# Performance work log

Measured on AMD Instinct MI355X. Metric: run time of the kernel, lower is better.

Reference implementation:

```python
import jax, jax.numpy as jnp
import numpy as np

B, S, H = 4, 1024, 1024
NH = 16
DH = H // NH  # 64


def setup_inputs() -> dict:
    key = jax.random.key(0)
    ks = jax.random.split(key, 8)
    std = 1.0 / np.sqrt(H)
    return {
        "query": jax.random.normal(ks[0], (B, S, H), jnp.float32),
        "key": jax.random.normal(ks[1], (B, S, H), jnp.float32),
        "value": jax.random.normal(ks[2], (B, S, H), jnp.float32),
        "masks": jnp.ones((B, S), jnp.float32),
        "Wq": jax.random.normal(ks[3], (H, H), jnp.float32) * std,
        "bq": jnp.zeros((H,), jnp.float32),
        "Wk": jax.random.normal(ks[4], (H, H), jnp.float32) * std,
        "bk": jnp.zeros((H,), jnp.float32),
        "Wv": jax.random.normal(ks[5], (H, H), jnp.float32) * std,
        "bv": jnp.zeros((H,), jnp.float32),
    }


def reference(query, key, value, masks, Wq, bq, Wk, bk, Wv, bv):
    # ReLU-gated projections (torch Linear: x @ W.T + b)
    qp = jax.nn.relu(jnp.einsum("bsh,oh->bso", query, Wq) + bq)
    kp = jax.nn.relu(jnp.einsum("bsh,oh->bso", key, Wk) + bk)
    vp = jax.nn.relu(jnp.einsum("bsh,oh->bso", value, Wv) + bv)
    # chunk(dim=2)+cat(dim=0) == split hidden into (NH, DH) contiguous slices
    qh = qp.reshape(B, S, NH, DH)
    kh = kp.reshape(B, S, NH, DH)
    vh = vp.reshape(B, S, NH, DH)
    scale = 1.0 / jnp.sqrt(jnp.asarray(DH, qp.dtype))
    # [B, NH, Sq, Sk]
    alpha = jnp.einsum("bqnd,bknd->bnqk", qh, kh) * scale
    alpha = jax.nn.softmax(alpha, axis=-1)
    # post-softmax multiplicative mask, applied per QUERY position
    alpha = alpha * masks[:, None, :, None]
    hiddens = jnp.einsum("bnqk,bknd->bqnd", alpha, vh).reshape(B, S, H)
    return hiddens + query
```

## Files before the change

### kernel.cpp

```cpp
#include <hip/hip_runtime.h>


typedef __attribute__((ext_vector_type(8))) __bf16 bf16x8;
typedef __attribute__((ext_vector_type(4))) float f32x4;
typedef __attribute__((ext_vector_type(8))) unsigned short u16x8;
typedef __attribute__((ext_vector_type(4))) unsigned short u16x4;

#define XQ_OFF 0u
#define XK_OFF 4194304u
#define XV_OFF 8388608u
#define WQ_OFF 12582912u
#define WK_OFF 13631488u
#define WV_OFF 14680064u
#define QP_OFF 15728640u
#define KP_OFF 19922944u
#define VP_OFF 24117248u
#define VT_OFF 28311552u

__device__ __forceinline__ unsigned short f2bf(float f) {
  union { float f; unsigned int u; } c; c.f = f;
  return (unsigned short)((c.u + 0x7fffu + ((c.u >> 16) & 1u)) >> 16);
}

__global__ __launch_bounds__(256) void cvt_kernel(
    const float* __restrict__ q, const float* __restrict__ k, const float* __restrict__ v,
    const float* __restrict__ wq, const float* __restrict__ wk, const float* __restrict__ wv,
    unsigned short* __restrict__ ws) {
  const int z = blockIdx.y;
  const float* src; unsigned short* dst; int n;
  switch (z) {
    case 0: src = q;  dst = ws + XQ_OFF; n = 4194304; break;
    case 1: src = k;  dst = ws + XK_OFF; n = 4194304; break;
    case 2: src = v;  dst = ws + XV_OFF; n = 4194304; break;
    case 3: src = wq; dst = ws + WQ_OFF; n = 1048576; break;
    case 4: src = wk; dst = ws + WK_OFF; n = 1048576; break;
    default: src = wv; dst = ws + WV_OFF; n = 1048576; break;
  }
  const int i8 = (blockIdx.x * 256 + threadIdx.x) * 8;
  if (i8 >= n) return;
  const float4 f0 = *(const float4*)(src + i8);
  const float4 f1 = *(const float4*)(src + i8 + 4);
  u16x8 r;
  r[0] = f2bf(f0.x); r[1] = f2bf(f0.y); r[2] = f2bf(f0.z); r[3] = f2bf(f0.w);
  r[4] = f2bf(f1.x); r[5] = f2bf(f1.y); r[6] = f2bf(f1.z); r[7] = f2bf(f1.w);
  *(u16x8*)(dst + i8) = r;
}

__global__ __launch_bounds__(256) void proj_gemm(
    unsigned short* __restrict__ ws,
    const float* __restrict__ bq, const float* __restrict__ bk, const float* __restrict__ bv) {
  __shared__ unsigned short As[128 * 32];
  __shared__ unsigned short Bs[128 * 32];
  const int z = blockIdx.z;
  const unsigned short* X = ws + (z == 0 ? XQ_OFF : z == 1 ? XK_OFF : XV_OFF);
  const unsigned short* W = ws + (z == 0 ? WQ_OFF : z == 1 ? WK_OFF : WV_OFF);
  unsigned short* P = ws + (z == 0 ? QP_OFF : z == 1 ? KP_OFF : VP_OFF);
  const float* bias = z == 0 ? bq : z == 1 ? bk : bv;

  const int tid  = threadIdx.x;
  const int lane = tid & 63;
  const int w    = tid >> 6;
  const int quad = lane >> 4;
  const int l15  = lane & 15;
  const int wr = w >> 1, wc = w & 1;
  const int m0 = blockIdx.y * 128;
  const int n0 = blockIdx.x * 128;

  f32x4 acc[4][4];
#pragma unroll
  for (int i = 0; i < 4; ++i)
#pragma unroll
    for (int j = 0; j < 4; ++j) acc[i][j] = f32x4{0.f, 0.f, 0.f, 0.f};

  for (int kt = 0; kt < 32; ++kt) {
    const int k0 = kt * 32;
#pragma unroll
    for (int pass = 0; pass < 2; ++pass) {
      const int c   = pass * 256 + tid;
      const int row = c >> 2;
      const int kc  = (c & 3) * 8;
      const unsigned short* ga = X + (size_t)(m0 + row) * 1024 + k0 + kc;
      const unsigned short* gb = W + (size_t)(n0 + row) * 1024 + k0 + kc;
      unsigned short* la = &As[(pass * 256 + w * 64) * 8];
      unsigned short* lb = &Bs[(pass * 256 + w * 64) * 8];
      __builtin_amdgcn_global_load_lds((const __attribute__((address_space(1))) void*)ga,
                                       (__attribute__((address_space(3))) void*)la, 16, 0, 0);
      __builtin_amdgcn_global_load_lds((const __attribute__((address_space(1))) void*)gb,
                                       (__attribute__((address_space(3))) void*)lb, 16, 0, 0);
    }
    __syncthreads();
    bf16x8 af[4], bfv[4];
#pragma unroll
    for (int mi = 0; mi < 4; ++mi)
      af[mi] = *(const bf16x8*)&As[(wr * 64 + mi * 16 + l15) * 32 + quad * 8];
#pragma unroll
    for (int ni = 0; ni < 4; ++ni)
      bfv[ni] = *(const bf16x8*)&Bs[(wc * 64 + ni * 16 + l15) * 32 + quad * 8];
#pragma unroll
    for (int mi = 0; mi < 4; ++mi)
#pragma unroll
      for (int ni = 0; ni < 4; ++ni)
        acc[mi][ni] = __builtin_amdgcn_mfma_f32_16x16x32_bf16(af[mi], bfv[ni], acc[mi][ni], 0, 0, 0);
    __syncthreads();
  }
#pragma unroll
  for (int mi = 0; mi < 4; ++mi)
#pragma unroll
    for (int ni = 0; ni < 4; ++ni) {
      const int col = n0 + wc * 64 + ni * 16 + l15;
      const float bvv = bias[col];
      const int row0 = m0 + wr * 64 + mi * 16 + quad * 4;
#pragma unroll
      for (int r = 0; r < 4; ++r) {
        float v = acc[mi][ni][r] + bvv;
        v = v > 0.f ? v : 0.f;
        P[(size_t)(row0 + r) * 1024 + col] = f2bf(v);
      }
    }
}

__global__ __launch_bounds__(256) void vtrans_kernel(
    const unsigned short* __restrict__ VP, unsigned short* __restrict__ VT) {
  __shared__ unsigned short T[64 * 72];
  const int tid = threadIdx.x;
  const int bh = blockIdx.y;
  const int b = bh >> 4, h = bh & 15;
  const int s0 = blockIdx.x * 64;
  const int rr = tid >> 2;
  const int cc = (tid & 3) * 16;
  {
    const unsigned short* g = &VP[(size_t)(b * 1024 + s0 + rr) * 1024 + h * 64 + cc];
    *(u16x8*)&T[rr * 72 + cc]     = *(const u16x8*)g;
    *(u16x8*)&T[rr * 72 + cc + 8] = *(const u16x8*)(g + 8);
  }
  __syncthreads();
  {
    unsigned short o[16];
#pragma unroll
    for (int jj = 0; jj < 16; ++jj) {
      const int j = (jj + (tid & 3) * 4) & 15;
      o[j] = T[(cc + j) * 72 + rr];
    }
    unsigned short* g = &VT[(size_t)(bh * 64 + rr) * 1024 + s0 + cc];
    *(u16x8*)g       = *(const u16x8*)&o[0];
    *(u16x8*)(g + 8) = *(const u16x8*)&o[8];
  }
}

__global__ __launch_bounds__(256, 2) void attn_kernel(
    const unsigned short* __restrict__ QP, const unsigned short* __restrict__ KP,
    const unsigned short* __restrict__ VT, const float* __restrict__ masks,
    const float* __restrict__ query, float* __restrict__ out) {
  __shared__ unsigned short Kt[64 * 72];
  __shared__ unsigned short Vt[64 * 72];
  __shared__ unsigned short Pl[4][32 * 72];
  const int tid  = threadIdx.x;
  const int lane = tid & 63;
  const int w    = tid >> 6;
  const int quad = lane >> 4;
  const int l15  = lane & 15;
  const int b = blockIdx.z, h = blockIdx.y;
  const int q0w = blockIdx.x * 128 + w * 32;
  const size_t base = (size_t)b * 1024 * 1024;
  const int bh = b * 16 + h;

  bf16x8 qf[2][2];
#pragma unroll
  for (int mt = 0; mt < 2; ++mt)
#pragma unroll
    for (int kk = 0; kk < 2; ++kk)
      qf[mt][kk] = *(const bf16x8*)&QP[base + (size_t)(q0w + mt * 16 + l15) * 1024 +
                                       h * 64 + kk * 32 + quad * 8];

  f32x4 o[2][4];
  float lsum[2][4];
#pragma unroll
  for (int mt = 0; mt < 2; ++mt)
#pragma unroll
    for (int nd = 0; nd < 4; ++nd) o[mt][nd] = f32x4{0.f, 0.f, 0.f, 0.f};
#pragma unroll
  for (int mt = 0; mt < 2; ++mt)
#pragma unroll
    for (int r = 0; r < 4; ++r) lsum[mt][r] = 0.f;

  const int srow = tid >> 2;
  const int c0   = (tid & 3) * 16;
  const float cvt = 0.18033688011112042f;

  for (int kb = 0; kb < 16; ++kb) {
    const int key0 = kb * 64;
    {
      const unsigned short* gk = &KP[base + (size_t)(key0 + srow) * 1024 + h * 64 + c0];
      *(u16x8*)&Kt[srow * 72 + c0]     = *(const u16x8*)gk;
      *(u16x8*)&Kt[srow * 72 + c0 + 8] = *(const u16x8*)(gk + 8);
      const unsigned short* gv = &VT[(size_t)(bh * 64 + srow) * 1024 + key0 + c0];
      *(u16x8*)&Vt[srow * 72 + c0]     = *(const u16x8*)gv;
      *(u16x8*)&Vt[srow * 72 + c0 + 8] = *(const u16x8*)(gv + 8);
    }
    __syncthreads();

#pragma unroll
    for (int mt = 0; mt < 2; ++mt) {
      f32x4 s[4];
#pragma unroll
      for (int ni = 0; ni < 4; ++ni) s[ni] = f32x4{0.f, 0.f, 0.f, 0.f};
#pragma unroll
      for (int kk = 0; kk < 2; ++kk)
#pragma unroll
        for (int ni = 0; ni < 4; ++ni) {
          bf16x8 kf = *(const bf16x8*)&Kt[(ni * 16 + l15) * 72 + kk * 32 + quad * 8];
          s[ni] = __builtin_amdgcn_mfma_f32_16x16x32_bf16(qf[mt][kk], kf, s[ni], 0, 0, 0);
        }
#pragma unroll
      for (int ni = 0; ni < 4; ++ni)
#pragma unroll
        for (int r = 0; r < 4; ++r) {
          const float p = exp2f(s[ni][r] * cvt - 8.0f);
          Pl[w][(mt * 16 + quad * 4 + r) * 72 + ni * 16 + l15] = f2bf(p);
          lsum[mt][r] += p;
        }
    }

#pragma unroll
    for (int kk = 0; kk < 2; ++kk) {
      bf16x8 pa[2];
#pragma unroll
      for (int mt = 0; mt < 2; ++mt)
        pa[mt] = *(const bf16x8*)&Pl[w][(mt * 16 + l15) * 72 + kk * 32 + quad * 8];
#pragma unroll
      for (int nd = 0; nd < 4; ++nd) {
        bf16x8 vf = *(const bf16x8*)&Vt[(nd * 16 + l15) * 72 + kk * 32 + quad * 8];
#pragma unroll
        for (int mt = 0; mt < 2; ++mt)
          o[mt][nd] = __builtin_amdgcn_mfma_f32_16x16x32_bf16(pa[mt], vf, o[mt][nd], 0, 0, 0);
      }
    }
    __syncthreads();
  }

#pragma unroll
  for (int mt = 0; mt < 2; ++mt) {
#pragma unroll
    for (int r = 0; r < 4; ++r) {
      float rs = lsum[mt][r];
      rs += __shfl_xor(rs, 1);
      rs += __shfl_xor(rs, 2);
      rs += __shfl_xor(rs, 4);
      rs += __shfl_xor(rs, 8);
      const int row = q0w + mt * 16 + quad * 4 + r;
      const float scale = masks[b * 1024 + row] / rs;
#pragma unroll
      for (int nd = 0; nd < 4; ++nd) {
        const int col = h * 64 + nd * 16 + l15;
        const size_t gi = base + (size_t)row * 1024 + col;
        out[gi] = o[mt][nd][r] * scale + query[gi];
      }
    }
  }
}

extern "C" void kernel_launch(void* const* d_in, const int* in_sizes, int n_in,
                              void* d_out, int out_size, void* d_ws, size_t ws_size,
                              hipStream_t stream) {
  const float* q     = (const float*)d_in[0];
  const float* k     = (const float*)d_in[1];
  const float* v     = (const float*)d_in[2];
  const float* masks = (const float*)d_in[3];
  const float* Wq    = (const float*)d_in[4];
  const float* bq    = (const float*)d_in[5];
  const float* Wk    = (const float*)d_in[6];
  const float* bk    = (const float*)d_in[7];
  const float* Wv    = (const float*)d_in[8];
  const float* bv    = (const float*)d_in[9];
  float* out = (float*)d_out;
  unsigned short* ws = (unsigned short*)d_ws;

  cvt_kernel<<<dim3(2048, 6), 256, 0, stream>>>(q, k, v, Wq, Wk, Wv, ws);
  proj_gemm<<<dim3(8, 32, 3), 256, 0, stream>>>(ws, bq, bk, bv);
  vtrans_kernel<<<dim3(16, 64), 256, 0, stream>>>(ws + VP_OFF, ws + VT_OFF);
  attn_kernel<<<dim3(8, 16, 4), 256, 0, stream>>>(ws + QP_OFF, ws + KP_OFF, ws + VT_OFF,
                                                  masks, q, out);
}
```

Before: 205.5 us.

## Fuse V transpose into projection epilogue and swizzle attention K/V staging

The projection GEMM now stages its output tile in shared memory and writes coalesced 16-byte rows. For V it writes the tile directly in head-transposed layout, which removes the separate vtrans kernel and its extra global round trip. The attention kernel loads K and V tiles with global_load_lds into an XOR-swizzled unpadded layout and computes S transposed so P can be stored as packed 4-element vectors. It also simplifies the row-sum reduction and drops the 2-block occupancy hint. The cost is more shared memory in the GEMM and added index complexity.

```diff
diff --git a/kernel.cpp b/kernel.cpp
--- a/kernel.cpp
+++ b/kernel.cpp
@@ -14,8 +14,7 @@
 #define WV_OFF 14680064u
 #define QP_OFF 15728640u
 #define KP_OFF 19922944u
-#define VP_OFF 24117248u
-#define VT_OFF 28311552u
+#define VT_OFF 24117248u
 
 __device__ __forceinline__ unsigned short f2bf(float f) {
   union { float f; unsigned int u; } c; c.f = f;
@@ -49,12 +48,13 @@
 __global__ __launch_bounds__(256) void proj_gemm(
     unsigned short* __restrict__ ws,
     const float* __restrict__ bq, const float* __restrict__ bk, const float* __restrict__ bv) {
-  __shared__ unsigned short As[128 * 32];
-  __shared__ unsigned short Bs[128 * 32];
+  __shared__ unsigned short smem[18432];
+  unsigned short* As = smem;
+  unsigned short* Bs = smem + 4096;
   const int z = blockIdx.z;
   const unsigned short* X = ws + (z == 0 ? XQ_OFF : z == 1 ? XK_OFF : XV_OFF);
   const unsigned short* W = ws + (z == 0 ? WQ_OFF : z == 1 ? WK_OFF : WV_OFF);
-  unsigned short* P = ws + (z == 0 ? QP_OFF : z == 1 ? KP_OFF : VP_OFF);
+  unsigned short* P = ws + (z == 0 ? QP_OFF : z == 1 ? KP_OFF : VT_OFF);
   const float* bias = z == 0 ? bq : z == 1 ? bk : bv;
 
   const int tid  = threadIdx.x;
@@ -103,56 +103,63 @@
         acc[mi][ni] = __builtin_amdgcn_mfma_f32_16x16x32_bf16(af[mi], bfv[ni], acc[mi][ni], 0, 0, 0);
     __syncthreads();
   }
-#pragma unroll
-  for (int mi = 0; mi < 4; ++mi)
-#pragma unroll
-    for (int ni = 0; ni < 4; ++ni) {
-      const int col = n0 + wc * 64 + ni * 16 + l15;
-      const float bvv = bias[col];
-      const int row0 = m0 + wr * 64 + mi * 16 + quad * 4;
-#pragma unroll
-      for (int r = 0; r < 4; ++r) {
-        float v = acc[mi][ni][r] + bvv;
-        v = v > 0.f ? v : 0.f;
-        P[(size_t)(row0 + r) * 1024 + col] = f2bf(v);
-      }
-    }
-}
-
-__global__ __launch_bounds__(256) void vtrans_kernel(
-    const unsigned short* __restrict__ VP, unsigned short* __restrict__ VT) {
-  __shared__ unsigned short T[64 * 72];
-  const int tid = threadIdx.x;
-  const int bh = blockIdx.y;
-  const int b = bh >> 4, h = bh & 15;
-  const int s0 = blockIdx.x * 64;
-  const int rr = tid >> 2;
-  const int cc = (tid & 3) * 16;
-  {
-    const unsigned short* g = &VP[(size_t)(b * 1024 + s0 + rr) * 1024 + h * 64 + cc];
-    *(u16x8*)&T[rr * 72 + cc]     = *(const u16x8*)g;
-    *(u16x8*)&T[rr * 72 + cc + 8] = *(const u16x8*)(g + 8);
-  }
-  __syncthreads();
-  {
-    unsigned short o[16];
-#pragma unroll
-    for (int jj = 0; jj < 16; ++jj) {
-      const int j = (jj + (tid & 3) * 4) & 15;
-      o[j] = T[(cc + j) * 72 + rr];
-    }
-    unsigned short* g = &VT[(size_t)(bh * 64 + rr) * 1024 + s0 + cc];
-    *(u16x8*)g       = *(const u16x8*)&o[0];
-    *(u16x8*)(g + 8) = *(const u16x8*)&o[8];
-  }
-}
-
-__global__ __launch_bounds__(256, 2) void attn_kernel(
+
+  unsigned short* Tw = smem + w * 4608;
+  if (z != 2) {
+#pragma unroll
+    for (int mi = 0; mi < 4; ++mi)
+#pragma unroll
+      for (int ni = 0; ni < 4; ++ni) {
+        const float bvv = bias[n0 + wc * 64 + ni * 16 + l15];
+#pragma unroll
+        for (int r = 0; r < 4; ++r) {
+          float v = acc[mi][ni][r] + bvv;
+          v = v > 0.f ? v : 0.f;
+          Tw[(mi * 16 + quad * 4 + r) * 72 + ni * 16 + l15] = f2bf(v);
+        }
+      }
+    const int row0 = m0 + wr * 64;
+    const int colb = n0 + wc * 64;
+#pragma unroll
+    for (int i = 0; i < 8; ++i) {
+      const int rr = i * 8 + (lane >> 3);
+      const int cc = (lane & 7) * 8;
+      *(u16x8*)&P[(size_t)(row0 + rr) * 1024 + colb + cc] = *(const u16x8*)&Tw[rr * 72 + cc];
+    }
+  } else {
+#pragma unroll
+    for (int mi = 0; mi < 4; ++mi)
+#pragma unroll
+      for (int ni = 0; ni < 4; ++ni) {
+        const float bvv = bias[n0 + wc * 64 + ni * 16 + l15];
+        u16x4 pk;
+#pragma unroll
+        for (int r = 0; r < 4; ++r) {
+          float v = acc[mi][ni][r] + bvv;
+          v = v > 0.f ? v : 0.f;
+          pk[r] = f2bf(v);
+        }
+        *(u16x4*)&Tw[(ni * 16 + l15) * 72 + mi * 16 + quad * 4] = pk;
+      }
+    const int h2 = (n0 >> 6) + wc;
+    const int bb = m0 >> 10;
+    const int s0 = (m0 & 1023) + wr * 64;
+#pragma unroll
+    for (int i = 0; i < 8; ++i) {
+      const int rr = i * 8 + (lane >> 3);
+      const int cc = (lane & 7) * 8;
+      *(u16x8*)&P[((size_t)(bb * 16 + h2) * 64 + rr) * 1024 + s0 + cc] =
+          *(const u16x8*)&Tw[rr * 72 + cc];
+    }
+  }
+}
+
+__global__ __launch_bounds__(256) void attn_kernel(
     const unsigned short* __restrict__ QP, const unsigned short* __restrict__ KP,
     const unsigned short* __restrict__ VT, const float* __restrict__ masks,
     const float* __restrict__ query, float* __restrict__ out) {
-  __shared__ unsigned short Kt[64 * 72];
-  __shared__ unsigned short Vt[64 * 72];
+  __shared__ unsigned short Kt[64 * 64];
+  __shared__ unsigned short Vt[64 * 64];
   __shared__ unsigned short Pl[4][32 * 72];
   const int tid  = threadIdx.x;
   const int lane = tid & 63;
@@ -173,52 +180,64 @@
                                        h * 64 + kk * 32 + quad * 8];
 
   f32x4 o[2][4];
-  float lsum[2][4];
+  float lsum[2] = {0.f, 0.f};
 #pragma unroll
   for (int mt = 0; mt < 2; ++mt)
 #pragma unroll
     for (int nd = 0; nd < 4; ++nd) o[mt][nd] = f32x4{0.f, 0.f, 0.f, 0.f};
-#pragma unroll
-  for (int mt = 0; mt < 2; ++mt)
-#pragma unroll
-    for (int r = 0; r < 4; ++r) lsum[mt][r] = 0.f;
-
-  const int srow = tid >> 2;
-  const int c0   = (tid & 3) * 16;
+
+  const int r_st = lane >> 3;
+  const int pc   = lane & 7;
+  const int swz  = l15 & 7;
   const float cvt = 0.18033688011112042f;
 
   for (int kb = 0; kb < 16; ++kb) {
     const int key0 = kb * 64;
-    {
-      const unsigned short* gk = &KP[base + (size_t)(key0 + srow) * 1024 + h * 64 + c0];
-      *(u16x8*)&Kt[srow * 72 + c0]     = *(const u16x8*)gk;
-      *(u16x8*)&Kt[srow * 72 + c0 + 8] = *(const u16x8*)(gk + 8);
-      const unsigned short* gv = &VT[(size_t)(bh * 64 + srow) * 1024 + key0 + c0];
-      *(u16x8*)&Vt[srow * 72 + c0]     = *(const u16x8*)gv;
-      *(u16x8*)&Vt[srow * 72 + c0 + 8] = *(const u16x8*)(gv + 8);
+#pragma unroll
+    for (int t = 0; t < 2; ++t) {
+      const int rowk = (w * 2 + t) * 8 + r_st;
+      const int lc   = pc ^ (rowk & 7);
+      const unsigned short* gk = &KP[base + (size_t)(key0 + rowk) * 1024 + h * 64 + lc * 8];
+      const unsigned short* gv = &VT[((size_t)bh * 64 + rowk) * 1024 + key0 + lc * 8];
+      __builtin_amdgcn_global_load_lds((const __attribute__((address_space(1))) void*)gk,
+                                       (__attribute__((address_space(3))) void*)&Kt[(w * 2 + t) * 512],
+                                       16, 0, 0);
+      __builtin_amdgcn_global_load_lds((const __attribute__((address_space(1))) void*)gv,
+                                       (__attribute__((address_space(3))) void*)&Vt[(w * 2 + t) * 512],
+                                       16, 0, 0);
     }
     __syncthreads();
 
+    bf16x8 kf[2][4];
+#pragma unroll
+    for (int kk = 0; kk < 2; ++kk)
+#pragma unroll
+      for (int ni = 0; ni < 4; ++ni)
+        kf[kk][ni] = *(const bf16x8*)&Kt[(ni * 16 + l15) * 64 + ((kk * 4 + quad) ^ swz) * 8];
+
 #pragma unroll
     for (int mt = 0; mt < 2; ++mt) {
-      f32x4 s[4];
-#pragma unroll
-      for (int ni = 0; ni < 4; ++ni) s[ni] = f32x4{0.f, 0.f, 0.f, 0.f};
+      f32x4 st[4];
+#pragma unroll
+      for (int ni = 0; ni < 4; ++ni) st[ni] = f32x4{0.f, 0.f, 0.f, 0.f};
 #pragma unroll
       for (int kk = 0; kk < 2; ++kk)
 #pragma unroll
-        for (int ni = 0; ni < 4; ++ni) {
-          bf16x8 kf = *(const bf16x8*)&Kt[(ni * 16 + l15) * 72 + kk * 32 + quad * 8];
-          s[ni] = __builtin_amdgcn_mfma_f32_16x16x32_bf16(qf[mt][kk], kf, s[ni], 0, 0, 0);
+        for (int ni = 0; ni < 4; ++ni)
+          st[ni] = __builtin_amdgcn_mfma_f32_16x16x32_bf16(kf[kk][ni], qf[mt][kk], st[ni], 0, 0, 0);
+      float ls = 0.f;
+#pragma unroll
+      for (int ni = 0; ni < 4; ++ni) {
+        u16x4 pk;
+#pragma unroll
+        for (int r = 0; r < 4; ++r) {
+          const float p = exp2f(st[ni][r] * cvt - 8.0f);
+          ls += p;
+          pk[r] = f2bf(p);
         }
-#pragma unroll
-      for (int ni = 0; ni < 4; ++ni)
-#pragma unroll
-        for (int r = 0; r < 4; ++r) {
-          const float p = exp2f(s[ni][r] * cvt - 8.0f);
-          Pl[w][(mt * 16 + quad * 4 + r) * 72 + ni * 16 + l15] = f2bf(p);
-          lsum[mt][r] += p;
-        }
+        *(u16x4*)&Pl[w][(mt * 16 + l15) * 72 + ni * 16 + quad * 4] = pk;
+      }
+      lsum[mt] += ls;
     }
 
 #pragma unroll
@@ -229,7 +248,7 @@
         pa[mt] = *(const bf16x8*)&Pl[w][(mt * 16 + l15) * 72 + kk * 32 + quad * 8];
 #pragma unroll
       for (int nd = 0; nd < 4; ++nd) {
-        bf16x8 vf = *(const bf16x8*)&Vt[(nd * 16 + l15) * 72 + kk * 32 + quad * 8];
+        bf16x8 vf = *(const bf16x8*)&Vt[(nd * 16 + l15) * 64 + ((kk * 4 + quad) ^ swz) * 8];
 #pragma unroll
         for (int mt = 0; mt < 2; ++mt)
           o[mt][nd] = __builtin_amdgcn_mfma_f32_16x16x32_bf16(pa[mt], vf, o[mt][nd], 0, 0, 0);
@@ -240,15 +259,18 @@
 
 #pragma unroll
   for (int mt = 0; mt < 2; ++mt) {
+    lsum[mt] += __shfl_xor(lsum[mt], 16);
+    lsum[mt] += __shfl_xor(lsum[mt], 32);
+  }
+
+#pragma unroll
+  for (int mt = 0; mt < 2; ++mt)
 #pragma unroll
     for (int r = 0; r < 4; ++r) {
-      float rs = lsum[mt][r];
-      rs += __shfl_xor(rs, 1);
-      rs += __shfl_xor(rs, 2);
-      rs += __shfl_xor(rs, 4);
-      rs += __shfl_xor(rs, 8);
-      const int row = q0w + mt * 16 + quad * 4 + r;
-      const float scale = masks[b * 1024 + row] / rs;
+      const int rq = quad * 4 + r;
+      const float ls = __shfl(lsum[mt], (lane & 48) | rq);
+      const int row = q0w + mt * 16 + rq;
+      const float scale = masks[b * 1024 + row] / ls;
 #pragma unroll
       for (int nd = 0; nd < 4; ++nd) {
         const int col = h * 64 + nd * 16 + l15;
@@ -256,7 +278,6 @@
         out[gi] = o[mt][nd][r] * scale + query[gi];
       }
     }
-  }
 }
 
 extern "C" void kernel_launch(void* const* d_in, const int* in_sizes, int n_in,
@@ -277,7 +298,6 @@
 
   cvt_kernel<<<dim3(2048, 6), 256, 0, stream>>>(q, k, v, Wq, Wk, Wv, ws);
   proj_gemm<<<dim3(8, 32, 3), 256, 0, stream>>>(ws, bq, bk, bv);
-  vtrans_kernel<<<dim3(16, 64), 256, 0, stream>>>(ws + VP_OFF, ws + VT_OFF);
   attn_kernel<<<dim3(8, 16, 4), 256, 0, stream>>>(ws + QP_OFF, ws + KP_OFF, ws + VT_OFF,
                                                   masks, q, out);
 }
```

Measured after the change: 207.2 us. No clear change (+0.9%).
